# Kernel optimization log

Measured on AMD Instinct MI355X. Metric: run time of the kernel, lower is better.

Reference implementation:

```python
import jax, jax.numpy as jnp
import numpy as np

B, I, H, O = 32768, 128, 128, 32
DEPTH, ARITY = 5, 2


def _xavier(k, shape):
    fan_in, fan_out = shape[-2], shape[-1]
    s = (2.0 / (fan_in + fan_out)) ** 0.5
    return jax.random.normal(k, shape, jnp.float32) * s


def setup_inputs() -> dict:
    key = jax.random.key(0)
    ks = jax.random.split(key, 12)
    return {
        "z": jax.random.normal(ks[0], (B, 1, I), jnp.float32),
        "z2h_w": _xavier(ks[1], (I, H)), "z2h_b": jnp.zeros((H,), jnp.float32),
        "h2o_w": _xavier(ks[2], (H, O)), "h2o_b": jnp.zeros((O,), jnp.float32),
        # GRU gate weights packed as [3(=r,z,n), in, out]
        "anc_wi": _xavier(ks[3], (3, O, H)), "anc_wh": _xavier(ks[4], (3, H, H)),
        "anc_bi": jnp.zeros((3, H), jnp.float32), "anc_bh": jnp.zeros((3, H), jnp.float32),
        "frat_wi": _xavier(ks[5], (3, O, H)), "frat_wh": _xavier(ks[6], (3, H, H)),
        "frat_bi": jnp.zeros((3, H), jnp.float32), "frat_bh": jnp.zeros((3, H), jnp.float32),
        "ua_w": _xavier(ks[7], (H, H)), "ua_b": jnp.zeros((H,), jnp.float32),
        "uf_w": _xavier(ks[8], (H, H)), "uf_b": jnp.zeros((H,), jnp.float32),
        "depth": DEPTH, "arity": ARITY,
    }


def _gru(x, h, wi, wh, bi, bh):
    # x: [B,1,O], h: [B,1,H]; wi: [3,O,H], wh: [3,H,H]
    gi = jnp.einsum('bto,koh->kbth', x, wi) + bi[:, None, None, :]
    gh = jnp.einsum('bth,khg->kbtg', h, wh) + bh[:, None, None, :]
    r = jax.nn.sigmoid(gi[0] + gh[0])
    z = jax.nn.sigmoid(gi[1] + gh[1])
    n = jnp.tanh(gi[2] + r * gh[2])
    return (1 - z) * n + z * h


def reference(z, z2h_w, z2h_b, h2o_w, h2o_b,
              anc_wi, anc_wh, anc_bi, anc_bh,
              frat_wi, frat_wh, frat_bi, frat_bh,
              ua_w, ua_b, uf_w, uf_b, depth, arity):
    preds = []

    def rec(hidden_a, d):
        # per-node symbol prediction, written into tree.prediction in the original
        pred = hidden_a @ h2o_w + h2o_b          # [B,1,O]
        probs = jax.nn.softmax(pred, axis=2)
        preds.append(pred)
        if d == 0:
            return probs
        h_ai = _gru(probs, hidden_a, anc_wi, anc_wh, anc_bi, anc_bh)
        # first child consumes the ancestral hidden directly
        probs_f = rec(h_ai, d - 1)
        hidden_f = h_ai
        for _ in range(arity - 1):
            hidden_f = _gru(probs_f, hidden_f, frat_wi, frat_wh, frat_bi, frat_bh)
            hidden = jnp.tanh(hidden_f @ uf_w + uf_b + hidden_a @ ua_w + ua_b)
            probs_f = rec(hidden, d - 1)
        return probs

    hidden0 = z @ z2h_w + z2h_b                  # [B,1,H]
    rec(hidden0, depth)
    return jnp.stack(preds)                      # [n_nodes(preorder), B, 1, O]
```

## Files before the change

### kernel.cpp

```cpp
#include <hip/hip_runtime.h>
#include <cstddef>


#define BATCH 32768

typedef float f32x4 __attribute__((ext_vector_type(4)));
typedef short s16x8 __attribute__((ext_vector_type(8)));
typedef unsigned short u16;

__device__ __forceinline__ float bf2f(u16 u){unsigned x=((unsigned)u)<<16;return __builtin_bit_cast(float,x);}
__device__ __forceinline__ u16 f2bf(float f){unsigned u=__builtin_bit_cast(unsigned,f);u+=0x7fffu+((u>>16)&1u);return (u16)(u>>16);}
__device__ __forceinline__ float sigm(float x){return 1.f/(1.f+__expf(-x));}
__device__ __forceinline__ float tanhf_(float x){return 1.f-2.f/(__expf(2.f*x)+1.f);}
__device__ __forceinline__ f32x4 mf(s16x8 a,s16x8 b,f32x4 c){return __builtin_amdgcn_mfma_f32_16x16x32_bf16(a,b,c,0,0,0);}

__device__ __constant__ unsigned char SCHED[62] = {
 5,4,3,2,1,9,10,1,9,11,2,1,9,10,1,9,12,3,2,1,9,10,1,9,11,2,1,9,10,1,9,13,
 4,3,2,1,9,10,1,9,11,2,1,9,10,1,9,12,3,2,1,9,10,1,9,11,2,1,9,10,1,9};

__global__ void prep_kernel(const float* __restrict__ z2h_w, const float* __restrict__ h2o_w,
                            const float* __restrict__ anc_wi, const float* __restrict__ anc_wh,
                            const float* __restrict__ frat_wi, const float* __restrict__ frat_wh,
                            const float* __restrict__ ua_w, const float* __restrict__ uf_w,
                            const float* __restrict__ anc_bi, const float* __restrict__ anc_bh,
                            const float* __restrict__ frat_bi, const float* __restrict__ frat_bh,
                            const float* __restrict__ ua_b, const float* __restrict__ uf_b,
                            u16* __restrict__ Wz, u16* __restrict__ Wo, u16* __restrict__ Wanc,
                            u16* __restrict__ Wfrat, u16* __restrict__ Wu,
                            float* __restrict__ Bga, float* __restrict__ Bgf, float* __restrict__ Bu) {
  int tid = blockIdx.x * blockDim.x + threadIdx.x;
  int stride = gridDim.x * blockDim.x;
  for (int i = tid; i < 128 * 128; i += stride) {
    int n = i / 128, k = i % 128;
    Wz[n * 128 + k] = f2bf(z2h_w[k * 128 + n]);
  }
  for (int i = tid; i < 32 * 128; i += stride) {
    int n = i / 128, k = i % 128;
    Wo[n * 128 + k] = f2bf(h2o_w[k * 32 + n]);
  }
  for (int i = tid; i < 512 * 160; i += stride) {
    int n = i / 160, k = i % 160;
    float va, vf;
    if (n < 256) {
      int g = n >> 7, hcc = n & 127;
      if (k < 32) { va = anc_wi[g*32*128 + k*128 + hcc]; vf = frat_wi[g*32*128 + k*128 + hcc]; }
      else        { va = anc_wh[g*128*128 + (k-32)*128 + hcc]; vf = frat_wh[g*128*128 + (k-32)*128 + hcc]; }
    } else if (n < 384) {
      int hcc = n - 256;
      if (k < 32) { va = anc_wi[2*32*128 + k*128 + hcc]; vf = frat_wi[2*32*128 + k*128 + hcc]; }
      else        { va = 0.f; vf = 0.f; }
    } else {
      int hcc = n - 384;
      if (k < 32) { va = 0.f; vf = 0.f; }
      else        { va = anc_wh[2*128*128 + (k-32)*128 + hcc]; vf = frat_wh[2*128*128 + (k-32)*128 + hcc]; }
    }
    Wanc[i] = f2bf(va);
    Wfrat[i] = f2bf(vf);
  }
  for (int i = tid; i < 128 * 256; i += stride) {
    int n = i / 256, k = i % 256;
    float v = (k < 128) ? uf_w[k * 128 + n] : ua_w[(k - 128) * 128 + n];
    Wu[i] = f2bf(v);
  }
  for (int i = tid; i < 128; i += stride) {
    Bga[i]       = anc_bi[i]       + anc_bh[i];
    Bga[128 + i] = anc_bi[128 + i] + anc_bh[128 + i];
    Bga[256 + i] = anc_bi[256 + i];
    Bga[384 + i] = anc_bh[256 + i];
    Bgf[i]       = frat_bi[i]       + frat_bh[i];
    Bgf[128 + i] = frat_bi[128 + i] + frat_bh[128 + i];
    Bgf[256 + i] = frat_bi[256 + i];
    Bgf[384 + i] = frat_bh[256 + i];
    Bu[i] = uf_b[i] + ua_b[i];
  }
}

__global__ __launch_bounds__(512, 2) void tree_kernel(
    const float* __restrict__ z,
    const u16* __restrict__ Wz, const u16* __restrict__ Wo,
    const u16* __restrict__ Wanc, const u16* __restrict__ Wfrat, const u16* __restrict__ Wu,
    const float* __restrict__ Bga, const float* __restrict__ Bgf, const float* __restrict__ Bu,
    const float* __restrict__ z2h_b, const float* __restrict__ h2o_b,
    u16* __restrict__ Gb, float* __restrict__ out) {
  __shared__ u16 R[17408];
  __shared__ u16 PRs[15360];
  const int tid = threadIdx.x;
  const int w = tid >> 6, l = tid & 63, lr = l & 15, lq = l >> 4, lk = lq * 8;
  const int hc = 16 * w + lr;
  const size_t brow = (size_t)blockIdx.x * 64;
  const size_t GSTR = (size_t)BATCH * 128;

  s16x8 FA[15], FF[15], FU[8];
#pragma unroll
  for (int j = 0; j < 15; ++j) {
    const int gb = (j < 5) ? 0 : ((j < 10) ? 1 : ((j < 11) ? 2 : 3));
    const int ks = (j < 5) ? j : ((j < 10) ? (j - 5) : ((j < 11) ? 0 : (j - 10)));
    const size_t off = (size_t)(128 * gb + hc) * 160 + ks * 32 + lk;
    FA[j] = *(const s16x8*)&Wanc[off];
    FF[j] = *(const s16x8*)&Wfrat[off];
  }
#pragma unroll
  for (int ks = 0; ks < 8; ++ks) FU[ks] = *(const s16x8*)&Wu[(size_t)hc * 256 + ks * 32 + lk];
  const float ba0 = Bga[hc], ba1 = Bga[128 + hc], ba2 = Bga[256 + hc], ba3 = Bga[384 + hc];
  const float bf0 = Bgf[hc], bf1 = Bgf[128 + hc], bf2 = Bgf[256 + hc], bf3 = Bgf[384 + hc];
  const float bub = Bu[hc];
  const float bz = z2h_b[hc];
  const float bo0 = h2o_b[lr], bo1 = h2o_b[16 + lr];

  int a1 = 0, h2 = 8704;

  auto pred_phase = [&](int node, int levC, bool doG, u16* Gdst, int hb, bool wantSM) {
    if (w >= 4) {
      const int m = w - 4;
      f32x4 p0 = {}, p1 = {};
#pragma unroll
      for (int ks = 0; ks < 4; ++ks) {
        s16x8 a = *(const s16x8*)&R[hb + (16 * m + lr) * 136 + ks * 32 + lk];
        s16x8 b0 = *(const s16x8*)&Wo[(size_t)lr * 128 + ks * 32 + lk];
        s16x8 b1 = *(const s16x8*)&Wo[(size_t)(16 + lr) * 128 + ks * 32 + lk];
        p0 = mf(a, b0, p0);
        p1 = mf(a, b1, p1);
      }
      float* op = out + ((size_t)node * BATCH + brow) * 32;
#pragma unroll
      for (int r = 0; r < 4; ++r) {
        int row = 16 * m + lq * 4 + r;
        float v0 = p0[r] + bo0, v1 = p1[r] + bo1;
        __builtin_nontemporal_store(v0, &op[row * 32 + lr]);
        __builtin_nontemporal_store(v1, &op[row * 32 + 16 + lr]);
        if (wantSM) {
          float mx = fmaxf(v0, v1);
#pragma unroll
          for (int o = 1; o < 16; o <<= 1) mx = fmaxf(mx, __shfl_xor(mx, o));
          float e0 = __expf(v0 - mx), e1 = __expf(v1 - mx);
          float s = e0 + e1;
#pragma unroll
          for (int o = 1; o < 16; o <<= 1) s += __shfl_xor(s, o);
          float inv = 1.f / s;
          PRs[levC * 2560 + row * 40 + lr] = f2bf(e0 * inv);
          PRs[levC * 2560 + row * 40 + 16 + lr] = f2bf(e1 * inv);
        }
      }
    } else if (doG) {
#pragma unroll
      for (int j = 0; j < 4; ++j) {
        int chunk = (w * 64 + l) + 256 * j, row = chunk >> 4, co = (chunk & 15) * 8;
        *(s16x8*)&Gdst[(brow + row) * 128 + co] = *(const s16x8*)&R[hb + row * 136 + co];
      }
    }
  };

  {
    int row = tid >> 3, seg = tid & 7;
    const float* src = z + (brow + row) * 128 + seg * 16;
    u16* dst = &R[a1 + row * 136 + seg * 16];
#pragma unroll
    for (int k = 0; k < 16; ++k) dst[k] = f2bf(src[k]);
  }
  __syncthreads();
  {
    f32x4 acc0[4] = {};
#pragma unroll
    for (int ks = 0; ks < 4; ++ks) {
      s16x8 b = *(const s16x8*)&Wz[(size_t)hc * 128 + ks * 32 + lk];
      s16x8 a[4];
#pragma unroll
      for (int mt = 0; mt < 4; ++mt) a[mt] = *(const s16x8*)&R[a1 + (16 * mt + lr) * 136 + ks * 32 + lk];
#pragma unroll
      for (int mt = 0; mt < 4; ++mt) acc0[mt] = mf(a[mt], b, acc0[mt]);
    }
#pragma unroll
    for (int mt = 0; mt < 4; ++mt)
#pragma unroll
      for (int r = 0; r < 4; ++r) {
        int row = 16 * mt + lq * 4 + r;
        R[h2 + row * 136 + hc] = f2bf(acc0[mt][r] + bz);
      }
  }
  __syncthreads();
  pred_phase(0, 5, true, Gb + 4 * GSTR, h2, true);
  __syncthreads();
  { int t = a1; a1 = h2; h2 = t; }

  for (int i = 0; i < 62; ++i) {
    const int sc = SCHED[i];
    const int lev = sc & 7;
    const bool isF = (sc & 8) != 0;
    const int node = i + 1;
    u16* Glm1 = Gb + (size_t)((lev >= 2) ? (lev - 2) : 0) * GSTR;
    u16* Glv  = Gb + (size_t)(lev - 1) * GSTR;

    if (!isF) {
#pragma unroll
      for (int half = 0; half < 2; ++half) {
        f32x4 acc[4][2] = {};
        {
          s16x8 a[2];
#pragma unroll
          for (int m2 = 0; m2 < 2; ++m2)
            a[m2] = *(const s16x8*)&PRs[lev * 2560 + (16 * (2 * half + m2) + lr) * 40 + lk];
#pragma unroll
          for (int m2 = 0; m2 < 2; ++m2) {
            acc[0][m2] = mf(a[m2], FA[0], acc[0][m2]);
            acc[1][m2] = mf(a[m2], FA[5], acc[1][m2]);
            acc[2][m2] = mf(a[m2], FA[10], acc[2][m2]);
          }
        }
#pragma unroll
        for (int ks = 1; ks < 5; ++ks) {
          s16x8 a[2];
#pragma unroll
          for (int m2 = 0; m2 < 2; ++m2)
            a[m2] = *(const s16x8*)&R[a1 + (16 * (2 * half + m2) + lr) * 136 + (ks - 1) * 32 + lk];
#pragma unroll
          for (int m2 = 0; m2 < 2; ++m2) {
            acc[0][m2] = mf(a[m2], FA[ks], acc[0][m2]);
            acc[1][m2] = mf(a[m2], FA[5 + ks], acc[1][m2]);
            acc[3][m2] = mf(a[m2], FA[10 + ks], acc[3][m2]);
          }
        }
#pragma unroll
        for (int m2 = 0; m2 < 2; ++m2)
#pragma unroll
          for (int r = 0; r < 4; ++r) {
            int row = 16 * (2 * half + m2) + lq * 4 + r;
            float rr = sigm(acc[0][m2][r] + ba0);
            float zz = sigm(acc[1][m2][r] + ba1);
            float nn = tanhf_(acc[2][m2][r] + ba2 + rr * (acc[3][m2][r] + ba3));
            float hold = bf2f(R[a1 + row * 136 + hc]);
            R[h2 + row * 136 + hc] = f2bf((1.f - zz) * nn + zz * hold);
          }
      }
      __syncthreads();
      pred_phase(node, lev - 1, lev >= 2, Glm1, h2, true);
      __syncthreads();
    } else {
      s16x8 hstage[2];
#pragma unroll
      for (int j = 0; j < 2; ++j) {
        int chunk = tid * 2 + j, row = chunk >> 4, co = (chunk & 15) * 8;
        hstage[j] = *(const s16x8*)&Glv[(brow + row) * 128 + co];
      }
      if (lev >= 2) {
#pragma unroll
        for (int j = 0; j < 2; ++j) {
          int chunk = tid * 2 + j, row = chunk >> 4, co = (chunk & 15) * 8;
          *(s16x8*)&R[a1 + row * 136 + co] = *(const s16x8*)&Glm1[(brow + row) * 128 + co];
        }
      }
      __syncthreads();
      u16 hfbuf[16];
#pragma unroll
      for (int half = 0; half < 2; ++half) {
        f32x4 acc[4][2] = {};
        {
          s16x8 a[2];
#pragma unroll
          for (int m2 = 0; m2 < 2; ++m2)
            a[m2] = *(const s16x8*)&PRs[(lev - 1) * 2560 + (16 * (2 * half + m2) + lr) * 40 + lk];
#pragma unroll
          for (int m2 = 0; m2 < 2; ++m2) {
            acc[0][m2] = mf(a[m2], FF[0], acc[0][m2]);
            acc[1][m2] = mf(a[m2], FF[5], acc[1][m2]);
            acc[2][m2] = mf(a[m2], FF[10], acc[2][m2]);
          }
        }
#pragma unroll
        for (int ks = 1; ks < 5; ++ks) {
          s16x8 a[2];
#pragma unroll
          for (int m2 = 0; m2 < 2; ++m2)
            a[m2] = *(const s16x8*)&R[a1 + (16 * (2 * half + m2) + lr) * 136 + (ks - 1) * 32 + lk];
#pragma unroll
          for (int m2 = 0; m2 < 2; ++m2) {
            acc[0][m2] = mf(a[m2], FF[ks], acc[0][m2]);
            acc[1][m2] = mf(a[m2], FF[5 + ks], acc[1][m2]);
            acc[3][m2] = mf(a[m2], FF[10 + ks], acc[3][m2]);
          }
        }
#pragma unroll
        for (int m2 = 0; m2 < 2; ++m2)
#pragma unroll
          for (int r = 0; r < 4; ++r) {
            int row = 16 * (2 * half + m2) + lq * 4 + r;
            float rr = sigm(acc[0][m2][r] + bf0);
            float zz = sigm(acc[1][m2][r] + bf1);
            float nn = tanhf_(acc[2][m2][r] + bf2 + rr * (acc[3][m2][r] + bf3));
            float hold = bf2f(R[a1 + row * 136 + hc]);
            hfbuf[(2 * half + m2) * 4 + r] = f2bf((1.f - zz) * nn + zz * hold);
          }
      }
      __syncthreads();
#pragma unroll
      for (int mt = 0; mt < 4; ++mt)
#pragma unroll
        for (int r = 0; r < 4; ++r) {
          int row = 16 * mt + lq * 4 + r;
          R[row * 264 + hc] = hfbuf[mt * 4 + r];
        }
#pragma unroll
      for (int j = 0; j < 2; ++j) {
        int chunk = tid * 2 + j, row = chunk >> 4, co = (chunk & 15) * 8;
        *(s16x8*)&R[row * 264 + 128 + co] = hstage[j];
      }
      __syncthreads();
      f32x4 acc2[4] = {};
#pragma unroll
      for (int ks = 0; ks < 8; ++ks) {
        s16x8 a[4];
#pragma unroll
        for (int mt = 0; mt < 4; ++mt) a[mt] = *(const s16x8*)&R[(16 * mt + lr) * 264 + ks * 32 + lk];
#pragma unroll
        for (int mt = 0; mt < 4; ++mt) acc2[mt] = mf(a[mt], FU[ks], acc2[mt]);
      }
      __syncthreads();
#pragma unroll
      for (int mt = 0; mt < 4; ++mt)
#pragma unroll
        for (int r = 0; r < 4; ++r) {
          int row = 16 * mt + lq * 4 + r;
          R[h2 + row * 136 + hc] = f2bf(tanhf_(acc2[mt][r] + bub));
        }
      __syncthreads();
      pred_phase(node, lev - 1, lev >= 2, Glm1, h2, lev >= 2);
      __syncthreads();
    }
    { int t = a1; a1 = h2; h2 = t; }
  }
}

extern "C" void kernel_launch(void* const* d_in, const int* in_sizes, int n_in,
                              void* d_out, int out_size, void* d_ws, size_t ws_size,
                              hipStream_t stream) {
  const float* z       = (const float*)d_in[0];
  const float* z2h_w   = (const float*)d_in[1];
  const float* z2h_b   = (const float*)d_in[2];
  const float* h2o_w   = (const float*)d_in[3];
  const float* h2o_b   = (const float*)d_in[4];
  const float* anc_wi  = (const float*)d_in[5];
  const float* anc_wh  = (const float*)d_in[6];
  const float* anc_bi  = (const float*)d_in[7];
  const float* anc_bh  = (const float*)d_in[8];
  const float* frat_wi = (const float*)d_in[9];
  const float* frat_wh = (const float*)d_in[10];
  const float* frat_bi = (const float*)d_in[11];
  const float* frat_bh = (const float*)d_in[12];
  const float* ua_w    = (const float*)d_in[13];
  const float* ua_b    = (const float*)d_in[14];
  const float* uf_w    = (const float*)d_in[15];
  const float* uf_b    = (const float*)d_in[16];
  (void)in_sizes; (void)n_in; (void)out_size; (void)ws_size;

  char* ws = (char*)d_ws;
  u16* Wz    = (u16*)(ws + 0);
  u16* Wo    = (u16*)(ws + 32768);
  u16* Wanc  = (u16*)(ws + 40960);
  u16* Wfrat = (u16*)(ws + 204800);
  u16* Wu    = (u16*)(ws + 368640);
  float* Bga = (float*)(ws + 434176);
  float* Bgf = (float*)(ws + 436224);
  float* Bu  = (float*)(ws + 438272);
  u16* Gb    = (u16*)(ws + 524288);
  float* out = (float*)d_out;

  hipLaunchKernelGGL(prep_kernel, dim3(256), dim3(256), 0, stream,
                     z2h_w, h2o_w, anc_wi, anc_wh, frat_wi, frat_wh, ua_w, uf_w,
                     anc_bi, anc_bh, frat_bi, frat_bh, ua_b, uf_b,
                     Wz, Wo, Wanc, Wfrat, Wu, Bga, Bgf, Bu);

  hipLaunchKernelGGL(tree_kernel, dim3(BATCH / 64), dim3(512), 0, stream,
                     z, Wz, Wo, Wanc, Wfrat, Wu, Bga, Bgf, Bu, z2h_b, h2o_b,
                     Gb, out);
}
```

Before: 1.421 ms.

## Double rows per block to 128 and reload Wu weights per fraternal step

Each block now processes 128 batch rows instead of 64, so the register-resident GRU weight fragments are reused over twice as many rows and the grid halves to 256 blocks. Shared memory doubles to about 130 KB. The Wu fragments are no longer kept in registers for the whole kernel; they are loaded from global memory at each fraternal step to free registers. The z load is vectorised and the h_f and staged hidden states are packed into the existing R buffers instead of a separate 264-stride layout. The risks are lower occupancy from the larger LDS footprint and fewer blocks than CUs on the device.

```diff
diff --git a/kernel.cpp b/kernel.cpp
--- a/kernel.cpp
+++ b/kernel.cpp
@@ -3,6 +3,11 @@
 
 
 #define BATCH 32768
+#define ROWS 128
+#define NBLK (BATCH / ROWS)
+#define RSTR 136
+#define HB2 17408
+#define PRL 5120
 
 typedef float f32x4 __attribute__((ext_vector_type(4)));
 typedef short s16x8 __attribute__((ext_vector_type(8)));
@@ -75,22 +80,23 @@
   }
 }
 
-__global__ __launch_bounds__(512, 2) void tree_kernel(
+__global__ __launch_bounds__(512) __attribute__((amdgpu_waves_per_eu(2, 2)))
+void tree_kernel(
     const float* __restrict__ z,
     const u16* __restrict__ Wz, const u16* __restrict__ Wo,
     const u16* __restrict__ Wanc, const u16* __restrict__ Wfrat, const u16* __restrict__ Wu,
     const float* __restrict__ Bga, const float* __restrict__ Bgf, const float* __restrict__ Bu,
     const float* __restrict__ z2h_b, const float* __restrict__ h2o_b,
     u16* __restrict__ Gb, float* __restrict__ out) {
-  __shared__ u16 R[17408];
-  __shared__ u16 PRs[15360];
+  __shared__ __align__(16) u16 R[34816];
+  __shared__ __align__(16) u16 PRs[30720];
   const int tid = threadIdx.x;
   const int w = tid >> 6, l = tid & 63, lr = l & 15, lq = l >> 4, lk = lq * 8;
   const int hc = 16 * w + lr;
-  const size_t brow = (size_t)blockIdx.x * 64;
+  const size_t brow = (size_t)blockIdx.x * ROWS;
   const size_t GSTR = (size_t)BATCH * 128;
 
-  s16x8 FA[15], FF[15], FU[8];
+  s16x8 FA[15], FF[15];
 #pragma unroll
   for (int j = 0; j < 15; ++j) {
     const int gb = (j < 5) ? 0 : ((j < 10) ? 1 : ((j < 11) ? 2 : 3));
@@ -99,82 +105,102 @@
     FA[j] = *(const s16x8*)&Wanc[off];
     FF[j] = *(const s16x8*)&Wfrat[off];
   }
-#pragma unroll
-  for (int ks = 0; ks < 8; ++ks) FU[ks] = *(const s16x8*)&Wu[(size_t)hc * 256 + ks * 32 + lk];
   const float ba0 = Bga[hc], ba1 = Bga[128 + hc], ba2 = Bga[256 + hc], ba3 = Bga[384 + hc];
   const float bf0 = Bgf[hc], bf1 = Bgf[128 + hc], bf2 = Bgf[256 + hc], bf3 = Bgf[384 + hc];
   const float bub = Bu[hc];
   const float bz = z2h_b[hc];
   const float bo0 = h2o_b[lr], bo1 = h2o_b[16 + lr];
 
-  int a1 = 0, h2 = 8704;
+  int a1 = 0, h2 = HB2;
 
   auto pred_phase = [&](int node, int levC, bool doG, u16* Gdst, int hb, bool wantSM) {
     if (w >= 4) {
-      const int m = w - 4;
-      f32x4 p0 = {}, p1 = {};
-#pragma unroll
-      for (int ks = 0; ks < 4; ++ks) {
-        s16x8 a = *(const s16x8*)&R[hb + (16 * m + lr) * 136 + ks * 32 + lk];
-        s16x8 b0 = *(const s16x8*)&Wo[(size_t)lr * 128 + ks * 32 + lk];
-        s16x8 b1 = *(const s16x8*)&Wo[(size_t)(16 + lr) * 128 + ks * 32 + lk];
-        p0 = mf(a, b0, p0);
-        p1 = mf(a, b1, p1);
-      }
+      const int wm = w - 4;
+      s16x8 b0 = *(const s16x8*)&Wo[(size_t)lr * 128 + lk];
+      s16x8 b1 = *(const s16x8*)&Wo[(size_t)(16 + lr) * 128 + lk];
+      s16x8 b0b = *(const s16x8*)&Wo[(size_t)lr * 128 + 32 + lk];
+      s16x8 b1b = *(const s16x8*)&Wo[(size_t)(16 + lr) * 128 + 32 + lk];
+      s16x8 b0c = *(const s16x8*)&Wo[(size_t)lr * 128 + 64 + lk];
+      s16x8 b1c = *(const s16x8*)&Wo[(size_t)(16 + lr) * 128 + 64 + lk];
+      s16x8 b0d = *(const s16x8*)&Wo[(size_t)lr * 128 + 96 + lk];
+      s16x8 b1d = *(const s16x8*)&Wo[(size_t)(16 + lr) * 128 + 96 + lk];
       float* op = out + ((size_t)node * BATCH + brow) * 32;
 #pragma unroll
-      for (int r = 0; r < 4; ++r) {
-        int row = 16 * m + lq * 4 + r;
-        float v0 = p0[r] + bo0, v1 = p1[r] + bo1;
-        __builtin_nontemporal_store(v0, &op[row * 32 + lr]);
-        __builtin_nontemporal_store(v1, &op[row * 32 + 16 + lr]);
-        if (wantSM) {
-          float mx = fmaxf(v0, v1);
-#pragma unroll
-          for (int o = 1; o < 16; o <<= 1) mx = fmaxf(mx, __shfl_xor(mx, o));
-          float e0 = __expf(v0 - mx), e1 = __expf(v1 - mx);
-          float s = e0 + e1;
-#pragma unroll
-          for (int o = 1; o < 16; o <<= 1) s += __shfl_xor(s, o);
-          float inv = 1.f / s;
-          PRs[levC * 2560 + row * 40 + lr] = f2bf(e0 * inv);
-          PRs[levC * 2560 + row * 40 + 16 + lr] = f2bf(e1 * inv);
+      for (int t = 0; t < 2; ++t) {
+        const int mt = 2 * wm + t;
+        f32x4 p0 = {}, p1 = {};
+        {
+          s16x8 a0 = *(const s16x8*)&R[hb + (16 * mt + lr) * RSTR + lk];
+          s16x8 a1f = *(const s16x8*)&R[hb + (16 * mt + lr) * RSTR + 32 + lk];
+          s16x8 a2f = *(const s16x8*)&R[hb + (16 * mt + lr) * RSTR + 64 + lk];
+          s16x8 a3f = *(const s16x8*)&R[hb + (16 * mt + lr) * RSTR + 96 + lk];
+          p0 = mf(a0, b0, p0); p1 = mf(a0, b1, p1);
+          p0 = mf(a1f, b0b, p0); p1 = mf(a1f, b1b, p1);
+          p0 = mf(a2f, b0c, p0); p1 = mf(a2f, b1c, p1);
+          p0 = mf(a3f, b0d, p0); p1 = mf(a3f, b1d, p1);
+        }
+#pragma unroll
+        for (int r = 0; r < 4; ++r) {
+          int row = 16 * mt + lq * 4 + r;
+          float v0 = p0[r] + bo0, v1 = p1[r] + bo1;
+          __builtin_nontemporal_store(v0, &op[row * 32 + lr]);
+          __builtin_nontemporal_store(v1, &op[row * 32 + 16 + lr]);
+          if (wantSM) {
+            float mx = fmaxf(v0, v1);
+#pragma unroll
+            for (int o = 1; o < 16; o <<= 1) mx = fmaxf(mx, __shfl_xor(mx, o));
+            float e0 = __expf(v0 - mx), e1 = __expf(v1 - mx);
+            float s = e0 + e1;
+#pragma unroll
+            for (int o = 1; o < 16; o <<= 1) s += __shfl_xor(s, o);
+            float inv = 1.f / s;
+            PRs[levC * PRL + row * 40 + lr] = f2bf(e0 * inv);
+            PRs[levC * PRL + row * 40 + 16 + lr] = f2bf(e1 * inv);
+          }
         }
       }
     } else if (doG) {
 #pragma unroll
-      for (int j = 0; j < 4; ++j) {
+      for (int j = 0; j < 8; ++j) {
         int chunk = (w * 64 + l) + 256 * j, row = chunk >> 4, co = (chunk & 15) * 8;
-        *(s16x8*)&Gdst[(brow + row) * 128 + co] = *(const s16x8*)&R[hb + row * 136 + co];
+        *(s16x8*)&Gdst[(brow + row) * 128 + co] = *(const s16x8*)&R[hb + row * RSTR + co];
       }
     }
   };
 
   {
-    int row = tid >> 3, seg = tid & 7;
-    const float* src = z + (brow + row) * 128 + seg * 16;
-    u16* dst = &R[a1 + row * 136 + seg * 16];
-#pragma unroll
-    for (int k = 0; k < 16; ++k) dst[k] = f2bf(src[k]);
+    int row = tid >> 2, seg = tid & 3;
+    const float* src = z + (brow + row) * 128 + seg * 32;
+    u16 tmp[32];
+#pragma unroll
+    for (int q = 0; q < 8; ++q) {
+      float4 v = *(const float4*)(src + 4 * q);
+      tmp[4*q] = f2bf(v.x); tmp[4*q+1] = f2bf(v.y); tmp[4*q+2] = f2bf(v.z); tmp[4*q+3] = f2bf(v.w);
+    }
+#pragma unroll
+    for (int q = 0; q < 4; ++q)
+      *(s16x8*)&R[a1 + row * RSTR + seg * 32 + q * 8] = *(const s16x8*)&tmp[q * 8];
   }
   __syncthreads();
-  {
+#pragma unroll
+  for (int half = 0; half < 2; ++half) {
     f32x4 acc0[4] = {};
 #pragma unroll
     for (int ks = 0; ks < 4; ++ks) {
       s16x8 b = *(const s16x8*)&Wz[(size_t)hc * 128 + ks * 32 + lk];
       s16x8 a[4];
 #pragma unroll
-      for (int mt = 0; mt < 4; ++mt) a[mt] = *(const s16x8*)&R[a1 + (16 * mt + lr) * 136 + ks * 32 + lk];
-#pragma unroll
-      for (int mt = 0; mt < 4; ++mt) acc0[mt] = mf(a[mt], b, acc0[mt]);
+      for (int m4 = 0; m4 < 4; ++m4)
+        a[m4] = *(const s16x8*)&R[a1 + (16 * (4 * half + m4) + lr) * RSTR + ks * 32 + lk];
+#pragma unroll
+      for (int m4 = 0; m4 < 4; ++m4) acc0[m4] = mf(a[m4], b, acc0[m4]);
     }
 #pragma unroll
-    for (int mt = 0; mt < 4; ++mt)
+    for (int m4 = 0; m4 < 4; ++m4)
 #pragma unroll
       for (int r = 0; r < 4; ++r) {
-        int row = 16 * mt + lq * 4 + r;
-        R[h2 + row * 136 + hc] = f2bf(acc0[mt][r] + bz);
+        int row = 16 * (4 * half + m4) + lq * 4 + r;
+        R[h2 + row * RSTR + hc] = f2bf(acc0[m4][r] + bz);
       }
   }
   __syncthreads();
@@ -192,13 +218,13 @@
 
     if (!isF) {
 #pragma unroll
-      for (int half = 0; half < 2; ++half) {
+      for (int hg = 0; hg < 4; ++hg) {
         f32x4 acc[4][2] = {};
         {
           s16x8 a[2];
 #pragma unroll
           for (int m2 = 0; m2 < 2; ++m2)
-            a[m2] = *(const s16x8*)&PRs[lev * 2560 + (16 * (2 * half + m2) + lr) * 40 + lk];
+            a[m2] = *(const s16x8*)&PRs[lev * PRL + (16 * (2 * hg + m2) + lr) * 40 + lk];
 #pragma unroll
           for (int m2 = 0; m2 < 2; ++m2) {
             acc[0][m2] = mf(a[m2], FA[0], acc[0][m2]);
@@ -211,7 +237,7 @@
           s16x8 a[2];
 #pragma unroll
           for (int m2 = 0; m2 < 2; ++m2)
-            a[m2] = *(const s16x8*)&R[a1 + (16 * (2 * half + m2) + lr) * 136 + (ks - 1) * 32 + lk];
+            a[m2] = *(const s16x8*)&R[a1 + (16 * (2 * hg + m2) + lr) * RSTR + (ks - 1) * 32 + lk];
 #pragma unroll
           for (int m2 = 0; m2 < 2; ++m2) {
             acc[0][m2] = mf(a[m2], FA[ks], acc[0][m2]);
@@ -223,41 +249,47 @@
         for (int m2 = 0; m2 < 2; ++m2)
 #pragma unroll
           for (int r = 0; r < 4; ++r) {
-            int row = 16 * (2 * half + m2) + lq * 4 + r;
+            int row = 16 * (2 * hg + m2) + lq * 4 + r;
             float rr = sigm(acc[0][m2][r] + ba0);
             float zz = sigm(acc[1][m2][r] + ba1);
             float nn = tanhf_(acc[2][m2][r] + ba2 + rr * (acc[3][m2][r] + ba3));
-            float hold = bf2f(R[a1 + row * 136 + hc]);
-            R[h2 + row * 136 + hc] = f2bf((1.f - zz) * nn + zz * hold);
+            float hold = bf2f(R[a1 + row * RSTR + hc]);
+            R[h2 + row * RSTR + hc] = f2bf((1.f - zz) * nn + zz * hold);
           }
       }
       __syncthreads();
       pred_phase(node, lev - 1, lev >= 2, Glm1, h2, true);
       __syncthreads();
     } else {
-      s16x8 hstage[2];
-#pragma unroll
-      for (int j = 0; j < 2; ++j) {
-        int chunk = tid * 2 + j, row = chunk >> 4, co = (chunk & 15) * 8;
+      s16x8 hstage[4];
+#pragma unroll
+      for (int j = 0; j < 4; ++j) {
+        int chunk = tid + 512 * j, row = chunk >> 4, co = (chunk & 15) * 8;
         hstage[j] = *(const s16x8*)&Glv[(brow + row) * 128 + co];
       }
       if (lev >= 2) {
-#pragma unroll
-        for (int j = 0; j < 2; ++j) {
-          int chunk = tid * 2 + j, row = chunk >> 4, co = (chunk & 15) * 8;
-          *(s16x8*)&R[a1 + row * 136 + co] = *(const s16x8*)&Glm1[(brow + row) * 128 + co];
-        }
-      }
-      __syncthreads();
-      u16 hfbuf[16];
-#pragma unroll
-      for (int half = 0; half < 2; ++half) {
+        s16x8 st[4];
+#pragma unroll
+        for (int j = 0; j < 4; ++j) {
+          int chunk = tid + 512 * j, row = chunk >> 4, co = (chunk & 15) * 8;
+          st[j] = *(const s16x8*)&Glm1[(brow + row) * 128 + co];
+        }
+#pragma unroll
+        for (int j = 0; j < 4; ++j) {
+          int chunk = tid + 512 * j, row = chunk >> 4, co = (chunk & 15) * 8;
+          *(s16x8*)&R[a1 + row * RSTR + co] = st[j];
+        }
+      }
+      __syncthreads();
+      unsigned hfp[16];
+#pragma unroll
+      for (int hg = 0; hg < 4; ++hg) {
         f32x4 acc[4][2] = {};
         {
           s16x8 a[2];
 #pragma unroll
           for (int m2 = 0; m2 < 2; ++m2)
-            a[m2] = *(const s16x8*)&PRs[(lev - 1) * 2560 + (16 * (2 * half + m2) + lr) * 40 + lk];
+            a[m2] = *(const s16x8*)&PRs[(lev - 1) * PRL + (16 * (2 * hg + m2) + lr) * 40 + lk];
 #pragma unroll
           for (int m2 = 0; m2 < 2; ++m2) {
             acc[0][m2] = mf(a[m2], FF[0], acc[0][m2]);
@@ -270,7 +302,7 @@
           s16x8 a[2];
 #pragma unroll
           for (int m2 = 0; m2 < 2; ++m2)
-            a[m2] = *(const s16x8*)&R[a1 + (16 * (2 * half + m2) + lr) * 136 + (ks - 1) * 32 + lk];
+            a[m2] = *(const s16x8*)&R[a1 + (16 * (2 * hg + m2) + lr) * RSTR + (ks - 1) * 32 + lk];
 #pragma unroll
           for (int m2 = 0; m2 < 2; ++m2) {
             acc[0][m2] = mf(a[m2], FF[ks], acc[0][m2]);
@@ -279,48 +311,74 @@
           }
         }
 #pragma unroll
-        for (int m2 = 0; m2 < 2; ++m2)
+        for (int m2 = 0; m2 < 2; ++m2) {
+          unsigned pk0 = 0, pk1 = 0;
 #pragma unroll
           for (int r = 0; r < 4; ++r) {
-            int row = 16 * (2 * half + m2) + lq * 4 + r;
+            int row = 16 * (2 * hg + m2) + lq * 4 + r;
             float rr = sigm(acc[0][m2][r] + bf0);
             float zz = sigm(acc[1][m2][r] + bf1);
             float nn = tanhf_(acc[2][m2][r] + bf2 + rr * (acc[3][m2][r] + bf3));
-            float hold = bf2f(R[a1 + row * 136 + hc]);
-            hfbuf[(2 * half + m2) * 4 + r] = f2bf((1.f - zz) * nn + zz * hold);
-          }
-      }
-      __syncthreads();
-#pragma unroll
-      for (int mt = 0; mt < 4; ++mt)
-#pragma unroll
-        for (int r = 0; r < 4; ++r) {
-          int row = 16 * mt + lq * 4 + r;
-          R[row * 264 + hc] = hfbuf[mt * 4 + r];
-        }
-#pragma unroll
-      for (int j = 0; j < 2; ++j) {
-        int chunk = tid * 2 + j, row = chunk >> 4, co = (chunk & 15) * 8;
-        *(s16x8*)&R[row * 264 + 128 + co] = hstage[j];
-      }
-      __syncthreads();
-      f32x4 acc2[4] = {};
-#pragma unroll
-      for (int ks = 0; ks < 8; ++ks) {
-        s16x8 a[4];
-#pragma unroll
-        for (int mt = 0; mt < 4; ++mt) a[mt] = *(const s16x8*)&R[(16 * mt + lr) * 264 + ks * 32 + lk];
-#pragma unroll
-        for (int mt = 0; mt < 4; ++mt) acc2[mt] = mf(a[mt], FU[ks], acc2[mt]);
-      }
-      __syncthreads();
-#pragma unroll
-      for (int mt = 0; mt < 4; ++mt)
-#pragma unroll
-        for (int r = 0; r < 4; ++r) {
-          int row = 16 * mt + lq * 4 + r;
-          R[h2 + row * 136 + hc] = f2bf(tanhf_(acc2[mt][r] + bub));
-        }
+            float hold = bf2f(R[a1 + row * RSTR + hc]);
+            unsigned bv = f2bf((1.f - zz) * nn + zz * hold);
+            if (r < 2) pk0 |= bv << (16 * (r & 1)); else pk1 |= bv << (16 * (r & 1));
+          }
+          hfp[(2 * hg + m2) * 2] = pk0;
+          hfp[(2 * hg + m2) * 2 + 1] = pk1;
+        }
+      }
+      s16x8 FUt[8];
+#pragma unroll
+      for (int ks = 0; ks < 8; ++ks) FUt[ks] = *(const s16x8*)&Wu[(size_t)hc * 256 + ks * 32 + lk];
+      __syncthreads();
+#pragma unroll
+      for (int i2 = 0; i2 < 16; ++i2) {
+        int mt = i2 >> 1, rr2 = (i2 & 1) * 2;
+        int row = 16 * mt + lq * 4 + rr2;
+        R[a1 + row * RSTR + hc] = (u16)(hfp[i2] & 0xffffu);
+        R[a1 + (row + 1) * RSTR + hc] = (u16)(hfp[i2] >> 16);
+      }
+#pragma unroll
+      for (int j = 0; j < 4; ++j) {
+        int chunk = tid + 512 * j, row = chunk >> 4, co = (chunk & 15) * 8;
+        *(s16x8*)&R[h2 + row * RSTR + co] = hstage[j];
+      }
+      __syncthreads();
+      unsigned h2p[16];
+#pragma unroll
+      for (int half = 0; half < 2; ++half) {
+        f32x4 acc2[4] = {};
+#pragma unroll
+        for (int ks = 0; ks < 8; ++ks) {
+          const int base = (ks < 4) ? a1 : h2;
+          const int ko = (ks & 3) * 32;
+          s16x8 a[4];
+#pragma unroll
+          for (int m4 = 0; m4 < 4; ++m4)
+            a[m4] = *(const s16x8*)&R[base + (16 * (4 * half + m4) + lr) * RSTR + ko + lk];
+#pragma unroll
+          for (int m4 = 0; m4 < 4; ++m4) acc2[m4] = mf(a[m4], FUt[ks], acc2[m4]);
+        }
+#pragma unroll
+        for (int m4 = 0; m4 < 4; ++m4) {
+          unsigned pk0 = 0, pk1 = 0;
+#pragma unroll
+          for (int r = 0; r < 4; ++r) {
+            unsigned bv = f2bf(tanhf_(acc2[m4][r] + bub));
+            if (r < 2) pk0 |= bv << (16 * (r & 1)); else pk1 |= bv << (16 * (r & 1));
+          }
+          h2p[(4 * half + m4) * 2] = pk0;
+          h2p[(4 * half + m4) * 2 + 1] = pk1;
+        }
+      }
+      __syncthreads();
+#pragma unroll
+      for (int i2 = 0; i2 < 16; ++i2) {
+        int mt = i2 >> 1, rr2 = (i2 & 1) * 2;
+        int row = 16 * mt + lq * 4 + rr2;
+        R[h2 + row * RSTR + hc] = (u16)(h2p[i2] & 0xffffu);
+        R[h2 + (row + 1) * RSTR + hc] = (u16)(h2p[i2] >> 16);
+      }
       __syncthreads();
       pred_phase(node, lev - 1, lev >= 2, Glm1, h2, lev >= 2);
       __syncthreads();
@@ -368,7 +426,7 @@
                      anc_bi, anc_bh, frat_bi, frat_bh, ua_b, uf_b,
                      Wz, Wo, Wanc, Wfrat, Wu, Bga, Bgf, Bu);
 
-  hipLaunchKernelGGL(tree_kernel, dim3(BATCH / 64), dim3(512), 0, stream,
+  hipLaunchKernelGGL(tree_kernel, dim3(NBLK), dim3(512), 0, stream,
                      z, Wz, Wo, Wanc, Wfrat, Wu, Bga, Bgf, Bu, z2h_b, h2o_b,
                      Gb, out);
 }
```

After: 1.517 ms. 6.8% more time.
